# Kernel optimization log

Hardware: AMD Instinct MI355X
Metric: run time of the kernel (lower is better)

The kernel has to match this reference:

```python
import jax, jax.numpy as jnp
import numpy as np

B, L, D = 4, 4096, 768
ORDER = 2
EMB = 33      # HyenaFilter emb_dim default
FFN = 64      # filter_order
FREQ = 10.0


def setup_inputs() -> dict:
    key = jax.random.key(0)
    ks = jax.random.split(key, 10)
    def rn(i, shape, scale):
        return jax.random.normal(ks[i], shape, dtype=jnp.float32) * scale
    return {
        "u": jax.random.normal(ks[0], (B, L, D), dtype=jnp.float32),
        "W_in": rn(1, (D, (ORDER + 1) * D), 0.02),
        "b_in": jnp.zeros(((ORDER + 1) * D,), jnp.float32),
        "conv_k": rn(2, (3, (ORDER + 1) * D), 0.3),   # depthwise kernel, 3 taps
        "conv_b": jnp.zeros(((ORDER + 1) * D,), jnp.float32),
        "W1": rn(3, (EMB, FFN), 0.1),
        "b1": jnp.zeros((FFN,), jnp.float32),
        "W2": rn(4, (FFN, ORDER * D), 0.05),
        "b2": jnp.zeros((ORDER * D,), jnp.float32),
        "f_bias": rn(5, (ORDER, D), 0.05),
        "f_decay": rn(6, (ORDER, D), 0.05),
        "W_out": rn(7, (D, D), 0.02),
        "b_out": jnp.zeros((D,), jnp.float32),
    }


def _hyena_filter(W1, b1, W2, b2, f_bias, f_decay):
    # Implicit filter: sinusoidal positional features -> MLP with sin activation
    t = jnp.linspace(0.0, 1.0, L)[:, None]                      # [L,1]
    bands = jnp.linspace(0.0, float(EMB - 1), EMB)[None, :]     # [1,EMB]
    pe = jnp.sin(t * bands * FREQ)                              # [L,EMB]
    h = jnp.sin(FREQ * (pe @ W1 + b1))                          # [L,FFN]
    h = h @ W2 + b2                                             # [L,ORDER*D]
    h = h.reshape(L, ORDER, D).transpose(1, 2, 0)               # [ORDER,D,L]
    t_window = jnp.linspace(0.0, float(L), L)[None, None, :]    # [1,1,L]
    decay = jnp.exp(-jnp.exp(f_decay)[:, :, None] * t_window)   # [ORDER,D,L]
    return h * decay + f_bias[:, :, None]


def reference(u, W_in, b_in, conv_k, conv_b, W1, b1, W2, b2,
              f_bias, f_decay, W_out, b_out):
    # input projection: [B,L,D] -> [B,L,(ORDER+1)*D]
    proj = u @ W_in + b_in
    # depthwise causal conv, kernel_size=3 (pad 2 on the left)
    xp = jnp.pad(proj, ((0, 0), (2, 0), (0, 0)))
    proj = (xp[:, 0:L, :] * conv_k[0]
            + xp[:, 1:L + 1, :] * conv_k[1]
            + xp[:, 2:L + 2, :] * conv_k[2]) + conv_b
    proj = proj.reshape(B, L, ORDER + 1, D).transpose(0, 2, 3, 1)  # [B,ORDER+1,D,L]
    x = proj[:, :ORDER]   # gates, [B,ORDER,D,L]
    v = proj[:, ORDER]    # value, [B,D,L]

    h = _hyena_filter(W1, b1, W2, b2, f_bias, f_decay)  # [ORDER,D,L]

    n_fft = 2 * L  # zero-padded linear convolution via rfft
    for n in range(ORDER):
        v_f = jnp.fft.rfft(v, n=n_fft, axis=-1)          # [B,D,L+1] complex
        h_f = jnp.fft.rfft(h[n], n=n_fft, axis=-1)       # [D,L+1] complex
        y = jnp.fft.irfft(v_f * h_f[None], n=n_fft, axis=-1)[..., :L]
        v = y * x[:, n]                                   # gated recurrence

    return v.transpose(0, 2, 1) @ W_out + b_out           # [B,L,D]
```

## Files before the change

### kernel.cpp

```cpp
#include <hip/hip_runtime.h>
#include <math.h>

#define L_SEQ 4096
#define D_DIM 768
#define C3    2304
#define TAPS  32

typedef __attribute__((ext_vector_type(8))) short bf16x8;
typedef __attribute__((ext_vector_type(4))) float f32x4;

__device__ __forceinline__ unsigned short f2bf(float x) {
  union { float f; unsigned u; } v; v.f = x;
  unsigned r = v.u + 0x7FFF + ((v.u >> 16) & 1);
  return (unsigned short)(r >> 16);
}
__device__ __forceinline__ float bf2f(unsigned short u) {
  union { unsigned u; float f; } v; v.u = ((unsigned)u) << 16; return v.f;
}
__device__ __forceinline__ void gld_lds16(const void* g, void* l) {
  __builtin_amdgcn_global_load_lds((const __attribute__((address_space(1))) void*)g,
                                   (__attribute__((address_space(3))) void*)l, 16, 0, 0);
}

__global__ __launch_bounds__(256) void filt_kernel(const float* __restrict__ W1,
                                                   const float* __restrict__ b1,
                                                   const float* __restrict__ W2,
                                                   const float* __restrict__ b2,
                                                   const float* __restrict__ f_decay,
                                                   float* __restrict__ g_tab) {
  __shared__ float phi_s[2048];
  const int tid = threadIdx.x;
  #pragma unroll
  for (int it = 0; it < 8; ++it) {
    int idx = tid + it * 256;
    int t = idx >> 6, f = idx & 63;
    float tt = (float)t / 4095.0f;
    float s = b1[f];
    #pragma unroll
    for (int e = 0; e < 33; ++e)
      s += sinf(tt * (float)e * 10.0f) * W1[e * 64 + f];
    phi_s[idx] = sinf(10.0f * s);
  }
  __syncthreads();
  int idx = blockIdx.x * 256 + tid;
  int c2 = idx >> 5, t = idx & 31;
  float acc = b2[c2];
  #pragma unroll 8
  for (int f = 0; f < 64; ++f)
    acc += phi_s[t * 64 + f] * W2[f * 1536 + c2];
  float r = expf(f_decay[c2]);
  g_tab[idx] = acc * expf(-r * (float)t * (4096.0f / 4095.0f));
}

__global__ __launch_bounds__(256) void cvt_kernel(const float* __restrict__ src,
                                                  unsigned short* __restrict__ dst) {
  int idx = (blockIdx.x * 256 + threadIdx.x) * 4;
  float4 v = *(const float4*)&src[idx];
  ushort4 o;
  o.x = f2bf(v.x); o.y = f2bf(v.y); o.z = f2bf(v.z); o.w = f2bf(v.w);
  *(ushort4*)&dst[idx] = o;
}

__global__ __launch_bounds__(256) void wtrans_kernel(const float* __restrict__ W_in,
                                                     unsigned short* __restrict__ W_inT,
                                                     const float* __restrict__ W_out,
                                                     unsigned short* __restrict__ W_outT) {
  __shared__ float t[32][33];
  const int z = blockIdx.z;
  const float* src = z ? W_out : W_in;
  unsigned short* dst = z ? W_outT : W_inT;
  const int C = z ? 768 : 2304;
  const int c0 = blockIdx.x * 32, r0 = blockIdx.y * 32;
  if (c0 >= C) return;
  const int tx = threadIdx.x & 31, ty = threadIdx.x >> 5;
  #pragma unroll
  for (int rr = 0; rr < 4; ++rr)
    t[ty + rr * 8][tx] = src[(long)(r0 + ty + rr * 8) * C + c0 + tx];
  __syncthreads();
  #pragma unroll
  for (int rr = 0; rr < 4; ++rr)
    dst[(long)(c0 + ty + rr * 8) * 768 + r0 + tx] = f2bf(t[tx][ty + rr * 8]);
}

__device__ __forceinline__ void g1_vmwait(int VM) {
  if (VM == 3)      asm volatile("s_waitcnt vmcnt(3)" ::: "memory");
  else if (VM == 0) asm volatile("s_waitcnt vmcnt(0)" ::: "memory");
}

template<bool STG, int VM>
__device__ __forceinline__ void g1_step(int scur, int sstg, int kt, char* smemc, int tid,
                                        int wmRow, int wn64, int fm, int csel,
                                        const unsigned short* aP, const unsigned short* bP,
                                        f32x4 (&acc)[4][4]) {
  const unsigned short* As = (const unsigned short*)(smemc + scur * 24576);
  const unsigned short* Bs = (const unsigned short*)(smemc + scur * 24576 + 16384);
  bf16x8 af[4], bfr[4];
  #pragma unroll
  for (int i = 0; i < 4; ++i) af[i]  = *(const bf16x8*)&As[(wmRow + i * 16 + fm) * 32 + csel];
  #pragma unroll
  for (int jj = 0; jj < 4; ++jj) bfr[jj] = *(const bf16x8*)&Bs[(wn64 + jj * 16 + fm) * 32 + csel];
  if (STG) {
    const unsigned short* ap = aP + (kt + 2) * 32;
    const unsigned short* bp = bP + (kt + 2) * 32;
    char* d = smemc + sstg * 24576 + tid * 16;
    gld_lds16(ap,         d);
    gld_lds16(ap + 98304, d + 8192);
    gld_lds16(bp,         d + 16384);
  }
  asm volatile("" ::: "memory");
  __builtin_amdgcn_s_barrier();
  __builtin_amdgcn_s_setprio(1);
  __builtin_amdgcn_sched_barrier(0);
  #pragma unroll
  for (int i = 0; i < 4; ++i)
    #pragma unroll
    for (int jj = 0; jj < 4; ++jj)
      acc[i][jj] = __builtin_amdgcn_mfma_f32_16x16x32_bf16(af[i], bfr[jj], acc[i][jj], 0, 0, 0);
  __builtin_amdgcn_sched_barrier(0);
  __builtin_amdgcn_s_setprio(0);
  g1_vmwait(VM);
  asm volatile("" ::: "memory");
  __builtin_amdgcn_s_barrier();
}

__global__ __launch_bounds__(512, 4) void gemm1_2ph(const unsigned short* __restrict__ A,
                                                    const unsigned short* __restrict__ Bt,
                                                    const float* __restrict__ bias,
                                                    unsigned short* __restrict__ proj) {
  extern __shared__ char smemc[];
  const int tid = threadIdx.x;
  const int w = tid >> 6, lane = tid & 63;
  const int id = blockIdx.x;
  const int x8 = id & 7, jb = id >> 3;
  const int mt = x8 * 8 + jb / 18, nt = jb % 18;
  const int m0 = mt * 256, n0 = nt * 128;
  const int wmRow = (w & 3) * 64, wn64 = (w >> 2) * 64;
  const int fm = lane & 15;
  const int csel = (((lane >> 4) ^ ((fm >> 1) & 3)) << 3);
  const int q_src = ((tid & 3) ^ ((tid >> 3) & 3)) * 8;
  const unsigned short* aP = A  + (size_t)(m0 + (tid >> 2)) * 768 + q_src;
  const unsigned short* bP = Bt + (size_t)(n0 + (tid >> 2)) * 768 + q_src;
  f32x4 acc[4][4] = {};

  #pragma unroll
  for (int kt = 0; kt < 2; ++kt) {
    char* d = smemc + kt * 24576 + tid * 16;
    const unsigned short* ap = aP + kt * 32;
    const unsigned short* bp = bP + kt * 32;
    gld_lds16(ap,         d);
    gld_lds16(ap + 98304, d + 8192);
    gld_lds16(bp,         d + 16384);
  }
  asm volatile("s_waitcnt vmcnt(3)" ::: "memory");
  asm volatile("" ::: "memory");
  __builtin_amdgcn_s_barrier();

  int scur = 0;
  #pragma unroll 1
  for (int kt = 0; kt < 22; ++kt) {
    int sstg = scur + 2; if (sstg >= 3) sstg -= 3;
    g1_step<true, 3>(scur, sstg, kt, smemc, tid, wmRow, wn64, fm, csel, aP, bP, acc);
    scur = (scur == 2) ? 0 : scur + 1;
  }
  {
    int sstg = scur + 2; if (sstg >= 3) sstg -= 3;
    g1_step<false, 0>(scur, sstg, 22, smemc, tid, wmRow, wn64, fm, csel, aP, bP, acc);
    scur = (scur == 2) ? 0 : scur + 1;
  }
  g1_step<false, -1>(scur, 0, 23, smemc, tid, wmRow, wn64, fm, csel, aP, bP, acc);

  const int b = m0 >> 12, l0 = m0 & 4095;
  float* fbuf = (float*)smemc + w * 1088;
  const int fk = lane >> 4;
  #pragma unroll
  for (int j2 = 0; j2 < 4; ++j2) {
    __syncthreads();
    #pragma unroll
    for (int i = 0; i < 4; ++i)
      *(f32x4*)&fbuf[fm * 68 + i * 16 + fk * 4] = acc[i][j2];
    __syncthreads();
    #pragma unroll
    for (int p = 0; p < 4; ++p) {
      int nl = p * 4 + fk;
      int c = n0 + wn64 + j2 * 16 + nl;
      float4 v = *(float4*)&fbuf[nl * 68 + fm * 4];
      float bb = bias[c];
      ushort4 o;
      o.x = f2bf(v.x + bb); o.y = f2bf(v.y + bb);
      o.z = f2bf(v.z + bb); o.w = f2bf(v.w + bb);
      *(ushort4*)&proj[((size_t)b * C3 + c) * L_SEQ + l0 + wmRow + fm * 4] = o;
    }
  }
}

#define G2_BUF 12288
__global__ __launch_bounds__(256) void gemm2_mfma(const unsigned short* __restrict__ A,
                                                  const unsigned short* __restrict__ Bt,
                                                  const float* __restrict__ bias,
                                                  float* __restrict__ out) {
  __shared__ __align__(16) char smem[24576];
  const int tid = threadIdx.x;
  const int w = tid >> 6, lane = tid & 63;
  const int lr = tid >> 2, lc = tid & 3;
  const int id = blockIdx.y * 6 + blockIdx.x;
  const int x8 = id & 7, j = id >> 3;
  const int m0 = (x8 * 32 + j / 6) * 64;
  const int n0 = (j % 6) * 128;
  const int wm = (w & 1) * 32, wn = (w >> 1) * 64;
  const int fm = lane & 15, fk = lane >> 4;
  f32x4 acc[2][4] = {};
  const unsigned short* Ag = A + (size_t)(m0 + lr) * 768 + lc * 8;
  const unsigned short* Bg = Bt + (size_t)(n0 + lr) * 768 + lc * 8;

  {
    char* dst = smem + tid * 16;
    gld_lds16(Ag,            dst);
    gld_lds16(Bg,            dst + 4096);
    gld_lds16(Bg + 64 * 768, dst + 8192);
  }
  for (int kk = 0; kk < 24; ++kk) {
    const int cur = (kk & 1) * G2_BUF;
    __syncthreads();
    if (kk < 23) {
      const int k0 = (kk + 1) * 32;
      char* dst = smem + ((kk + 1) & 1) * G2_BUF + tid * 16;
      gld_lds16(Ag + k0,            dst);
      gld_lds16(Bg + k0,            dst + 4096);
      gld_lds16(Bg + k0 + 64 * 768, dst + 8192);
    }
    const unsigned short* As = (const unsigned short*)(smem + cur);
    const unsigned short* Bs = As + 2048;
    bf16x8 af[2], bfr[4];
    #pragma unroll
    for (int i = 0; i < 2; ++i) af[i]  = *(const bf16x8*)&As[(wm + i * 16 + fm) * 32 + fk * 8];
    #pragma unroll
    for (int j2 = 0; j2 < 4; ++j2) bfr[j2] = *(const bf16x8*)&Bs[(wn + j2 * 16 + fm) * 32 + fk * 8];
    #pragma unroll
    for (int i = 0; i < 2; ++i)
      #pragma unroll
      for (int j2 = 0; j2 < 4; ++j2)
        acc[i][j2] = __builtin_amdgcn_mfma_f32_16x16x32_bf16(af[i], bfr[j2], acc[i][j2], 0, 0, 0);
  }

  float* fbuf = (float*)smem + w * 1088;
  const int nf = lane & 15, mq = lane >> 4;
  float4 bb4 = *(const float4*)&bias[n0 + wn + nf * 4];
  #pragma unroll
  for (int i = 0; i < 2; ++i) {
    __syncthreads();
    #pragma unroll
    for (int cg = 0; cg < 4; ++cg)
      #pragma unroll
      for (int r = 0; r < 4; ++r)
        fbuf[(fk * 4 + r) * 68 + cg * 16 + fm] = acc[i][cg][r];
    __syncthreads();
    #pragma unroll
    for (int pass = 0; pass < 4; ++pass) {
      int m_l = pass * 4 + mq;
      float4 v = *(float4*)&fbuf[m_l * 68 + nf * 4];
      v.x += bb4.x; v.y += bb4.y; v.z += bb4.z; v.w += bb4.w;
      *(float4*)&out[(size_t)(m0 + wm + i * 16 + m_l) * D_DIM + n0 + wn + nf * 4] = v;
    }
  }
}

__global__ __launch_bounds__(256) void row_kernel(const unsigned short* __restrict__ proj,
                                                  unsigned short* __restrict__ v2T,
                                                  const float* __restrict__ conv_k,
                                                  const float* __restrict__ conv_b,
                                                  const float* __restrict__ g_tab,
                                                  const float* __restrict__ f_bias) {
  __shared__ float buf0[4128];
  __shared__ float buf1[4128];
  __shared__ float sgs[2 * TAPS];
  __shared__ float wsum[4];
  __shared__ float bnd[3][4][2];
  const int tid = threadIdx.x;
  const int lane = tid & 63, w = tid >> 6;
  const int b = blockIdx.x / D_DIM, d = blockIdx.x % D_DIM;
  const int g = tid * 16;

  const unsigned short* rowV  = proj + ((size_t)b * C3 + 2 * D_DIM + d) * L_SEQ;
  const unsigned short* rowX0 = proj + ((size_t)b * C3 + d) * L_SEQ;
  const unsigned short* rowX1 = proj + ((size_t)b * C3 + D_DIM + d) * L_SEQ;

  float v[16], x0[16], x1[16];
  #pragma unroll
  for (int k = 0; k < 4; ++k) {
    ushort4 qv = *(const ushort4*)&rowV[g + k * 4];
    v[k * 4] = bf2f(qv.x); v[k * 4 + 1] = bf2f(qv.y); v[k * 4 + 2] = bf2f(qv.z); v[k * 4 + 3] = bf2f(qv.w);
    ushort4 q0 = *(const ushort4*)&rowX0[g + k * 4];
    x0[k * 4] = bf2f(q0.x); x0[k * 4 + 1] = bf2f(q0.y); x0[k * 4 + 2] = bf2f(q0.z); x0[k * 4 + 3] = bf2f(q0.w);
    ushort4 q1 = *(const ushort4*)&rowX1[g + k * 4];
    x1[k * 4] = bf2f(q1.x); x1[k * 4 + 1] = bf2f(q1.y); x1[k * 4 + 2] = bf2f(q1.z); x1[k * 4 + 3] = bf2f(q1.w);
  }

  if (tid < 32) {
    int ph = (tid & 15) * 258 + (tid >> 4);
    buf0[ph] = 0.f; buf1[ph] = 0.f;
  }
  if (tid < 64) sgs[tid] = g_tab[((size_t)((tid >> 5) * D_DIM + d)) * TAPS + (tid & 31)];
  if (lane == 63) {
    bnd[0][w][0] = v[14];  bnd[0][w][1] = v[15];
    bnd[1][w][0] = x0[14]; bnd[1][w][1] = x0[15];
    bnd[2][w][0] = x1[14]; bnd[2][w][1] = x1[15];
  }
  const int cv = 2 * D_DIM + d, cx0 = d, cx1 = D_DIM + d;
  const float kv0 = conv_k[cv],  kv1 = conv_k[C3 + cv],  kv2 = conv_k[2 * C3 + cv],  bv = conv_b[cv];
  const float ka0 = conv_k[cx0], ka1 = conv_k[C3 + cx0], ka2 = conv_k[2 * C3 + cx0], ba = conv_b[cx0];
  const float kb0 = conv_k[cx1], kb1 = conv_k[C3 + cx1], kb2 = conv_k[2 * C3 + cx1], bb = conv_b[cx1];
  const float fb0 = f_bias[d], fb1 = f_bias[D_DIM + d];
  __syncthreads();

  float vm1 = __shfl_up(v[15], 1),  vm2 = __shfl_up(v[14], 1);
  float am1 = __shfl_up(x0[15], 1), am2 = __shfl_up(x0[14], 1);
  float bm1 = __shfl_up(x1[15], 1), bm2 = __shfl_up(x1[14], 1);
  if (lane == 0) {
    if (w > 0) {
      vm2 = bnd[0][w-1][0]; vm1 = bnd[0][w-1][1];
      am2 = bnd[1][w-1][0]; am1 = bnd[1][w-1][1];
      bm2 = bnd[2][w-1][0]; bm1 = bnd[2][w-1][1];
    } else {
      vm1 = vm2 = am1 = am2 = bm1 = bm2 = 0.f;
    }
  }
  float r[16];
  r[0] = vm2 * kv0 + vm1 * kv1 + v[0] * kv2 + bv;
  r[1] = vm1 * kv0 + v[0] * kv1 + v[1] * kv2 + bv;
  #pragma unroll
  for (int i = 2; i < 16; ++i) r[i] = v[i-2] * kv0 + v[i-1] * kv1 + v[i] * kv2 + bv;
  {
    float t0 = am2 * ka0 + am1 * ka1 + x0[0] * ka2 + ba;
    float t1 = am1 * ka0 + x0[0] * ka1 + x0[1] * ka2 + ba;
    #pragma unroll
    for (int i = 15; i >= 2; --i) x0[i] = x0[i-2] * ka0 + x0[i-1] * ka1 + x0[i] * ka2 + ba;
    x0[0] = t0; x0[1] = t1;
  }
  {
    float t0 = bm2 * kb0 + bm1 * kb1 + x1[0] * kb2 + bb;
    float t1 = bm1 * kb0 + x1[0] * kb1 + x1[1] * kb2 + bb;
    #pragma unroll
    for (int i = 15; i >= 2; --i) x1[i] = x1[i-2] * kb0 + x1[i-1] * kb1 + x1[i] * kb2 + bb;
    x1[0] = t0; x1[1] = t1;
  }
  #pragma unroll
  for (int i = 0; i < 16; ++i) buf0[i * 258 + tid + 2] = r[i];
  __syncthreads();

  float h[32];
  #pragma unroll
  for (int j = 0; j < 32; ++j) h[j] = buf0[(j & 15) * 258 + tid + (j >> 4)];
  float p[16], run = 0.f;
  #pragma unroll
  for (int i = 0; i < 16; ++i) { run += r[i]; p[i] = run; }
  float s = run;
  #pragma unroll
  for (int off = 1; off < 64; off <<= 1) {
    float o = __shfl_up(s, off);
    if (lane >= off) s += o;
  }
  if (lane == 63) wsum[w] = s;
  __syncthreads();
  float woff = 0.f;
  #pragma unroll
  for (int k = 0; k < 4; ++k) if (k < w) woff += wsum[k];
  float excl = woff + s - run;
  float y0[16];
  #pragma unroll
  for (int i = 0; i < 16; ++i) {
    float a = fb0 * (excl + p[i]);
    #pragma unroll
    for (int t = 0; t < TAPS; ++t) {
      float vv = (t <= i) ? r[i - t] : h[32 + i - t];
      a += sgs[t] * vv;
    }
    y0[i] = a * x0[i];
  }
  #pragma unroll
  for (int i = 0; i < 16; ++i) buf1[i * 258 + tid + 2] = y0[i];
  __syncthreads();

  #pragma unroll
  for (int j = 0; j < 32; ++j) h[j] = buf1[(j & 15) * 258 + tid + (j >> 4)];
  run = 0.f;
  #pragma unroll
  for (int i = 0; i < 16; ++i) { run += y0[i]; p[i] = run; }
  s = run;
  #pragma unroll
  for (int off = 1; off < 64; off <<= 1) {
    float o = __shfl_up(s, off);
    if (lane >= off) s += o;
  }
  if (lane == 63) wsum[w] = s;
  __syncthreads();
  woff = 0.f;
  #pragma unroll
  for (int k = 0; k < 4; ++k) if (k < w) woff += wsum[k];
  excl = woff + s - run;
  unsigned short yout[16];
  #pragma unroll
  for (int i = 0; i < 16; ++i) {
    float a = fb1 * (excl + p[i]);
    #pragma unroll
    for (int t = 0; t < TAPS; ++t) {
      float vv = (t <= i) ? y0[i - t] : h[32 + i - t];
      a += sgs[TAPS + t] * vv;
    }
    yout[i] = f2bf(a * x1[i]);
  }
  unsigned short* outRow = v2T + ((size_t)b * D_DIM + d) * L_SEQ + g;
  *(ushort4*)&outRow[0]  = *(ushort4*)&yout[0];
  *(ushort4*)&outRow[4]  = *(ushort4*)&yout[4];
  *(ushort4*)&outRow[8]  = *(ushort4*)&yout[8];
  *(ushort4*)&outRow[12] = *(ushort4*)&yout[12];
}

__global__ __launch_bounds__(256) void transpose_v2(const unsigned short* __restrict__ src,
                                                    unsigned short* __restrict__ dst) {
  __shared__ unsigned short t[64][66];
  const int l0 = blockIdx.x * 64, d0 = blockIdx.y * 64, b = blockIdx.z;
  const int tx = threadIdx.x & 31, ty = threadIdx.x >> 5;
  const unsigned short* s = src + ((size_t)b * D_DIM + d0) * L_SEQ + l0;
  #pragma unroll
  for (int r = 0; r < 8; ++r) {
    int dd = ty + r * 8;
    *(ushort2*)&t[dd][tx * 2] = *(const ushort2*)&s[(size_t)dd * L_SEQ + tx * 2];
  }
  __syncthreads();
  unsigned short* q = dst + ((size_t)b * L_SEQ + l0) * D_DIM + d0;
  #pragma unroll
  for (int r = 0; r < 8; ++r) {
    int ll = ty + r * 8;
    ushort2 v; v.x = t[tx * 2][ll]; v.y = t[tx * 2 + 1][ll];
    *(ushort2*)&q[(size_t)ll * D_DIM + tx * 2] = v;
  }
}

extern "C" void kernel_launch(void* const* d_in, const int* in_sizes, int n_in,
                              void* d_out, int out_size, void* d_ws, size_t ws_size,
                              hipStream_t stream) {
  (void)in_sizes; (void)n_in; (void)out_size; (void)ws_size;
  const float* u       = (const float*)d_in[0];
  const float* W_in    = (const float*)d_in[1];
  const float* b_in    = (const float*)d_in[2];
  const float* conv_k  = (const float*)d_in[3];
  const float* conv_b  = (const float*)d_in[4];
  const float* W1      = (const float*)d_in[5];
  const float* b1      = (const float*)d_in[6];
  const float* W2      = (const float*)d_in[7];
  const float* b2      = (const float*)d_in[8];
  const float* f_bias  = (const float*)d_in[9];
  const float* f_decay = (const float*)d_in[10];
  const float* W_out   = (const float*)d_in[11];
  const float* b_out   = (const float*)d_in[12];
  float* out = (float*)d_out;

  unsigned short* proj  = (unsigned short*)d_ws;
  unsigned short* v2T   = proj + (size_t)4 * C3 * L_SEQ;
  unsigned short* ubf   = v2T + (size_t)4 * D_DIM * L_SEQ;
  unsigned short* v2F   = ubf;
  unsigned short* W_inT = ubf + (size_t)16384 * 768;
  unsigned short* W_outT= W_inT + (size_t)C3 * D_DIM;
  float* g_tab          = (float*)(W_outT + (size_t)D_DIM * D_DIM);

  static bool g1_attr = false;
  if (!g1_attr) {
    (void)hipFuncSetAttribute(reinterpret_cast<const void*>(gemm1_2ph),
                              hipFuncAttributeMaxDynamicSharedMemorySize, 73728);
    g1_attr = true;
  }

  filt_kernel<<<192, 256, 0, stream>>>(W1, b1, W2, b2, f_decay, g_tab);
  cvt_kernel<<<12288, 256, 0, stream>>>(u, ubf);
  wtrans_kernel<<<dim3(72, 24, 2), 256, 0, stream>>>(W_in, W_inT, W_out, W_outT);
  gemm1_2ph<<<1152, 512, 73728, stream>>>(ubf, W_inT, b_in, proj);
  row_kernel<<<3072, 256, 0, stream>>>(proj, v2T, conv_k, conv_b, g_tab, f_bias);
  transpose_v2<<<dim3(64, 12, 4), 256, 0, stream>>>(v2T, v2F);
  gemm2_mfma<<<dim3(6, 256), 256, 0, stream>>>(v2F, W_outT, b_out, out);
}
```

Baseline: 307.7 us.

## Unify both GEMMs on a shared 128x128 triple-buffered MFMA k-loop

```diff
diff --git a/kernel.cpp b/kernel.cpp
--- a/kernel.cpp
+++ b/kernel.cpp
@@ -82,30 +82,31 @@
     dst[(long)(c0 + ty + rr * 8) * 768 + r0 + tx] = f2bf(t[tx][ty + rr * 8]);
 }
 
-__device__ __forceinline__ void g1_vmwait(int VM) {
-  if (VM == 3)      asm volatile("s_waitcnt vmcnt(3)" ::: "memory");
+__device__ __forceinline__ void g_vmwait(int VM) {
+  if (VM == 4)      asm volatile("s_waitcnt vmcnt(4)" ::: "memory");
   else if (VM == 0) asm volatile("s_waitcnt vmcnt(0)" ::: "memory");
 }
 
 template<bool STG, int VM>
-__device__ __forceinline__ void g1_step(int scur, int sstg, int kt, char* smemc, int tid,
-                                        int wmRow, int wn64, int fm, int csel,
-                                        const unsigned short* aP, const unsigned short* bP,
-                                        f32x4 (&acc)[4][4]) {
-  const unsigned short* As = (const unsigned short*)(smemc + scur * 24576);
-  const unsigned short* Bs = (const unsigned short*)(smemc + scur * 24576 + 16384);
+__device__ __forceinline__ void g_step(int scur, int sstg, int kt, char* smemc, int tid,
+                                       int wm64, int wn64, int fm, int csel,
+                                       const unsigned short* aP, const unsigned short* bP,
+                                       f32x4 (&acc)[4][4]) {
+  const unsigned short* As = (const unsigned short*)(smemc + scur * 16384);
+  const unsigned short* Bs = (const unsigned short*)(smemc + scur * 16384 + 8192);
   bf16x8 af[4], bfr[4];
   #pragma unroll
-  for (int i = 0; i < 4; ++i) af[i]  = *(const bf16x8*)&As[(wmRow + i * 16 + fm) * 32 + csel];
+  for (int i = 0; i < 4; ++i) af[i]  = *(const bf16x8*)&As[(wm64 + i * 16 + fm) * 32 + csel];
   #pragma unroll
   for (int jj = 0; jj < 4; ++jj) bfr[jj] = *(const bf16x8*)&Bs[(wn64 + jj * 16 + fm) * 32 + csel];
   if (STG) {
     const unsigned short* ap = aP + (kt + 2) * 32;
     const unsigned short* bp = bP + (kt + 2) * 32;
-    char* d = smemc + sstg * 24576 + tid * 16;
+    char* d = smemc + sstg * 16384 + tid * 16;
     gld_lds16(ap,         d);
-    gld_lds16(ap + 98304, d + 8192);
-    gld_lds16(bp,         d + 16384);
+    gld_lds16(ap + 49152, d + 4096);
+    gld_lds16(bp,         d + 8192);
+    gld_lds16(bp + 49152, d + 12288);
   }
   asm volatile("" ::: "memory");
   __builtin_amdgcn_s_barrier();
@@ -118,56 +119,61 @@
       acc[i][jj] = __builtin_amdgcn_mfma_f32_16x16x32_bf16(af[i], bfr[jj], acc[i][jj], 0, 0, 0);
   __builtin_amdgcn_sched_barrier(0);
   __builtin_amdgcn_s_setprio(0);
-  g1_vmwait(VM);
+  g_vmwait(VM);
   asm volatile("" ::: "memory");
   __builtin_amdgcn_s_barrier();
 }
 
-__global__ __launch_bounds__(512, 4) void gemm1_2ph(const unsigned short* __restrict__ A,
-                                                    const unsigned short* __restrict__ Bt,
-                                                    const float* __restrict__ bias,
-                                                    unsigned short* __restrict__ proj) {
+__device__ __forceinline__ void g_kloop(char* smemc, int tid, int wm64, int wn64, int fm,
+                                        int csel, const unsigned short* aP,
+                                        const unsigned short* bP, f32x4 (&acc)[4][4]) {
+  #pragma unroll
+  for (int kt = 0; kt < 2; ++kt) {
+    char* d = smemc + kt * 16384 + tid * 16;
+    const unsigned short* ap = aP + kt * 32;
+    const unsigned short* bp = bP + kt * 32;
+    gld_lds16(ap,         d);
+    gld_lds16(ap + 49152, d + 4096);
+    gld_lds16(bp,         d + 8192);
+    gld_lds16(bp + 49152, d + 12288);
+  }
+  asm volatile("s_waitcnt vmcnt(4)" ::: "memory");
+  asm volatile("" ::: "memory");
+  __builtin_amdgcn_s_barrier();
+  int scur = 0;
+  #pragma unroll 1
+  for (int kt = 0; kt < 22; ++kt) {
+    int sstg = scur + 2; if (sstg >= 3) sstg -= 3;
+    g_step<true, 4>(scur, sstg, kt, smemc, tid, wm64, wn64, fm, csel, aP, bP, acc);
+    scur = (scur == 2) ? 0 : scur + 1;
+  }
+  {
+    int sstg = scur + 2; if (sstg >= 3) sstg -= 3;
+    g_step<false, 0>(scur, sstg, 22, smemc, tid, wm64, wn64, fm, csel, aP, bP, acc);
+    scur = (scur == 2) ? 0 : scur + 1;
+  }
+  g_step<false, -1>(scur, 0, 23, smemc, tid, wm64, wn64, fm, csel, aP, bP, acc);
+}
+
+__global__ __launch_bounds__(256, 3) void gemm1_k3(const unsigned short* __restrict__ A,
+                                                   const unsigned short* __restrict__ Bt,
+                                                   const float* __restrict__ bias,
+                                                   unsigned short* __restrict__ proj) {
   extern __shared__ char smemc[];
   const int tid = threadIdx.x;
   const int w = tid >> 6, lane = tid & 63;
   const int id = blockIdx.x;
   const int x8 = id & 7, jb = id >> 3;
-  const int mt = x8 * 8 + jb / 18, nt = jb % 18;
-  const int m0 = mt * 256, n0 = nt * 128;
-  const int wmRow = (w & 3) * 64, wn64 = (w >> 2) * 64;
+  const int mt = x8 * 16 + jb / 18, nt = jb % 18;
+  const int m0 = mt * 128, n0 = nt * 128;
+  const int wm64 = (w & 1) * 64, wn64 = (w >> 1) * 64;
   const int fm = lane & 15;
   const int csel = (((lane >> 4) ^ ((fm >> 1) & 3)) << 3);
   const int q_src = ((tid & 3) ^ ((tid >> 3) & 3)) * 8;
   const unsigned short* aP = A  + (size_t)(m0 + (tid >> 2)) * 768 + q_src;
   const unsigned short* bP = Bt + (size_t)(n0 + (tid >> 2)) * 768 + q_src;
   f32x4 acc[4][4] = {};
-
-  #pragma unroll
-  for (int kt = 0; kt < 2; ++kt) {
-    char* d = smemc + kt * 24576 + tid * 16;
-    const unsigned short* ap = aP + kt * 32;
-    const unsigned short* bp = bP + kt * 32;
-    gld_lds16(ap,         d);
-    gld_lds16(ap + 98304, d + 8192);
-    gld_lds16(bp,         d + 16384);
-  }
-  asm volatile("s_waitcnt vmcnt(3)" ::: "memory");
-  asm volatile("" ::: "memory");
-  __builtin_amdgcn_s_barrier();
-
-  int scur = 0;
-  #pragma unroll 1
-  for (int kt = 0; kt < 22; ++kt) {
-    int sstg = scur + 2; if (sstg >= 3) sstg -= 3;
-    g1_step<true, 3>(scur, sstg, kt, smemc, tid, wmRow, wn64, fm, csel, aP, bP, acc);
-    scur = (scur == 2) ? 0 : scur + 1;
-  }
-  {
-    int sstg = scur + 2; if (sstg >= 3) sstg -= 3;
-    g1_step<false, 0>(scur, sstg, 22, smemc, tid, wmRow, wn64, fm, csel, aP, bP, acc);
-    scur = (scur == 2) ? 0 : scur + 1;
-  }
-  g1_step<false, -1>(scur, 0, 23, smemc, tid, wmRow, wn64, fm, csel, aP, bP, acc);
+  g_kloop(smemc, tid, wm64, wn64, fm, csel, aP, bP, acc);
 
   const int b = m0 >> 12, l0 = m0 & 4095;
   float* fbuf = (float*)smemc + w * 1088;
@@ -188,65 +194,37 @@
       ushort4 o;
       o.x = f2bf(v.x + bb); o.y = f2bf(v.y + bb);
       o.z = f2bf(v.z + bb); o.w = f2bf(v.w + bb);
-      *(ushort4*)&proj[((size_t)b * C3 + c) * L_SEQ + l0 + wmRow + fm * 4] = o;
+      *(ushort4*)&proj[((size_t)b * C3 + c) * L_SEQ + l0 + wm64 + fm * 4] = o;
     }
   }
 }
 
-#define G2_BUF 12288
-__global__ __launch_bounds__(256) void gemm2_mfma(const unsigned short* __restrict__ A,
-                                                  const unsigned short* __restrict__ Bt,
-                                                  const float* __restrict__ bias,
-                                                  float* __restrict__ out) {
-  __shared__ __align__(16) char smem[24576];
+__global__ __launch_bounds__(256, 3) void gemm2_k3(const unsigned short* __restrict__ A,
+                                                   const unsigned short* __restrict__ Bt,
+                                                   const float* __restrict__ bias,
+                                                   float* __restrict__ out) {
+  extern __shared__ char smemc[];
   const int tid = threadIdx.x;
   const int w = tid >> 6, lane = tid & 63;
-  const int lr = tid >> 2, lc = tid & 3;
-  const int id = blockIdx.y * 6 + blockIdx.x;
-  const int x8 = id & 7, j = id >> 3;
-  const int m0 = (x8 * 32 + j / 6) * 64;
-  const int n0 = (j % 6) * 128;
-  const int wm = (w & 1) * 32, wn = (w >> 1) * 64;
-  const int fm = lane & 15, fk = lane >> 4;
-  f32x4 acc[2][4] = {};
-  const unsigned short* Ag = A + (size_t)(m0 + lr) * 768 + lc * 8;
-  const unsigned short* Bg = Bt + (size_t)(n0 + lr) * 768 + lc * 8;
-
-  {
-    char* dst = smem + tid * 16;
-    gld_lds16(Ag,            dst);
-    gld_lds16(Bg,            dst + 4096);
-    gld_lds16(Bg + 64 * 768, dst + 8192);
-  }
-  for (int kk = 0; kk < 24; ++kk) {
-    const int cur = (kk & 1) * G2_BUF;
-    __syncthreads();
-    if (kk < 23) {
-      const int k0 = (kk + 1) * 32;
-      char* dst = smem + ((kk + 1) & 1) * G2_BUF + tid * 16;
-      gld_lds16(Ag + k0,            dst);
-      gld_lds16(Bg + k0,            dst + 4096);
-      gld_lds16(Bg + k0 + 64 * 768, dst + 8192);
-    }
-    const unsigned short* As = (const unsigned short*)(smem + cur);
-    const unsigned short* Bs = As + 2048;
-    bf16x8 af[2], bfr[4];
-    #pragma unroll
-    for (int i = 0; i < 2; ++i) af[i]  = *(const bf16x8*)&As[(wm + i * 16 + fm) * 32 + fk * 8];
-    #pragma unroll
-    for (int j2 = 0; j2 < 4; ++j2) bfr[j2] = *(const bf16x8*)&Bs[(wn + j2 * 16 + fm) * 32 + fk * 8];
-    #pragma unroll
-    for (int i = 0; i < 2; ++i)
-      #pragma unroll
-      for (int j2 = 0; j2 < 4; ++j2)
-        acc[i][j2] = __builtin_amdgcn_mfma_f32_16x16x32_bf16(af[i], bfr[j2], acc[i][j2], 0, 0, 0);
-  }
-
-  float* fbuf = (float*)smem + w * 1088;
+  const int id = blockIdx.x;
+  const int x8 = id & 7, jb = id >> 3;
+  const int mt = x8 * 16 + jb / 6, nt = jb % 6;
+  const int m0 = mt * 128, n0 = nt * 128;
+  const int wm64 = (w & 1) * 64, wn64 = (w >> 1) * 64;
+  const int fm = lane & 15;
+  const int csel = (((lane >> 4) ^ ((fm >> 1) & 3)) << 3);
+  const int q_src = ((tid & 3) ^ ((tid >> 3) & 3)) * 8;
+  const unsigned short* aP = A  + (size_t)(m0 + (tid >> 2)) * 768 + q_src;
+  const unsigned short* bP = Bt + (size_t)(n0 + (tid >> 2)) * 768 + q_src;
+  f32x4 acc[4][4] = {};
+  g_kloop(smemc, tid, wm64, wn64, fm, csel, aP, bP, acc);
+
+  float* fbuf = (float*)smemc + w * 1088;
+  const int fk = lane >> 4;
   const int nf = lane & 15, mq = lane >> 4;
-  float4 bb4 = *(const float4*)&bias[n0 + wn + nf * 4];
-  #pragma unroll
-  for (int i = 0; i < 2; ++i) {
+  float4 bb4 = *(const float4*)&bias[n0 + wn64 + nf * 4];
+  #pragma unroll
+  for (int i = 0; i < 4; ++i) {
     __syncthreads();
     #pragma unroll
     for (int cg = 0; cg < 4; ++cg)
@@ -259,7 +237,7 @@
       int m_l = pass * 4 + mq;
       float4 v = *(float4*)&fbuf[m_l * 68 + nf * 4];
       v.x += bb4.x; v.y += bb4.y; v.z += bb4.z; v.w += bb4.w;
-      *(float4*)&out[(size_t)(m0 + wm + i * 16 + m_l) * D_DIM + n0 + wn + nf * 4] = v;
+      *(float4*)&out[(size_t)(m0 + wm64 + i * 16 + m_l) * D_DIM + n0 + wn64 + nf * 4] = v;
     }
   }
 }
@@ -463,18 +441,20 @@
   unsigned short* W_outT= W_inT + (size_t)C3 * D_DIM;
   float* g_tab          = (float*)(W_outT + (size_t)D_DIM * D_DIM);
 
-  static bool g1_attr = false;
-  if (!g1_attr) {
-    (void)hipFuncSetAttribute(reinterpret_cast<const void*>(gemm1_2ph),
-                              hipFuncAttributeMaxDynamicSharedMemorySize, 73728);
-    g1_attr = true;
+  static bool g_attr = false;
+  if (!g_attr) {
+    (void)hipFuncSetAttribute(reinterpret_cast<const void*>(gemm1_k3),
+                              hipFuncAttributeMaxDynamicSharedMemorySize, 49152);
+    (void)hipFuncSetAttribute(reinterpret_cast<const void*>(gemm2_k3),
+                              hipFuncAttributeMaxDynamicSharedMemorySize, 49152);
+    g_attr = true;
   }
 
   filt_kernel<<<192, 256, 0, stream>>>(W1, b1, W2, b2, f_decay, g_tab);
   cvt_kernel<<<12288, 256, 0, stream>>>(u, ubf);
   wtrans_kernel<<<dim3(72, 24, 2), 256, 0, stream>>>(W_in, W_inT, W_out, W_outT);
-  gemm1_2ph<<<1152, 512, 73728, stream>>>(ubf, W_inT, b_in, proj);
+  gemm1_k3<<<2304, 256, 49152, stream>>>(ubf, W_inT, b_in, proj);
   row_kernel<<<3072, 256, 0, stream>>>(proj, v2T, conv_k, conv_b, g_tab, f_bias);
   transpose_v2<<<dim3(64, 12, 4), 256, 0, stream>>>(v2T, v2F);
-  gemm2_mfma<<<dim3(6, 256), 256, 0, stream>>>(v2F, W_outT, b_out, out);
-}
+  gemm2_k3<<<768, 256, 49152, stream>>>(v2F, W_outT, b_out, out);
+}
```

Measured after the change: 289.5 us. 5.9% less time.
